# Kernel tuning notes

Measured on AMD Instinct MI355X. Metric: run time of the kernel, lower is better.

The kernel has to match this reference:

```python
import jax, jax.numpy as jnp
import numpy as np

B, S, D, H = 4, 2048, 1024, 16
DH = D // H  # attention head size = 64


def setup_inputs() -> dict:
    key = jax.random.key(0)
    ks = jax.random.split(key, 5)
    scale = 1.0 / np.sqrt(D)
    return {
        "hidden_states": jax.random.normal(ks[0], (B, S, D), dtype=jnp.float32),
        "attention_mask": jnp.zeros((B, 1, 1, S), dtype=jnp.float32),
        "Wq": jax.random.normal(ks[1], (D, D), dtype=jnp.float32) * scale,
        "bq": jnp.zeros((D,), dtype=jnp.float32),
        "Wk": jax.random.normal(ks[2], (D, D), dtype=jnp.float32) * scale,
        "bk": jnp.zeros((D,), dtype=jnp.float32),
        "Wv": jax.random.normal(ks[3], (D, D), dtype=jnp.float32) * scale,
        "bv": jnp.zeros((D,), dtype=jnp.float32),
    }


def _heads(x):
    # [B,S,D] -> [B,H,S,DH]
    return x.reshape(B, S, H, DH).transpose(0, 2, 1, 3)


def reference(hidden_states, attention_mask, Wq, bq, Wk, bk, Wv, bv):
    # QKV projections (nn.Linear: x @ W.T + b)
    q = _heads(hidden_states @ Wq.T + bq)
    k = _heads(hidden_states @ Wk.T + bk)
    v = _heads(hidden_states @ Wv.T + bv)
    # scaled dot-product attention, eval mode (no dropout, no head_mask)
    scores = jnp.einsum("bhqd,bhkd->bhqk", q, k) / np.sqrt(DH).astype(np.float32)
    scores = scores + attention_mask  # additive mask broadcast to [B,H,S,S]
    probs = jax.nn.softmax(scores, axis=-1)
    ctx = jnp.einsum("bhqk,bhkd->bhqd", probs, v)
    # [B,H,S,DH] -> [B,S,D]
    return ctx.transpose(0, 2, 1, 3).reshape(B, S, D)
```

## Files before the change

### kernel.cpp

```cpp
#include <hip/hip_runtime.h>

typedef float f32x4 __attribute__((ext_vector_type(4)));
typedef __bf16 bf16x8 __attribute__((ext_vector_type(8)));
typedef __bf16 bf16x4 __attribute__((ext_vector_type(4)));
typedef unsigned short u16;
typedef unsigned int u32;

#define SEQ 2048
#define DMODEL 1024
#define MTOT 8192
#define LOG2E 1.4426950408889634f
#define C1 0.18033688011112042f

__device__ __forceinline__ void gl_lds16(const void* g, void* l) {
  __builtin_amdgcn_global_load_lds(
      (const __attribute__((address_space(1))) u32*)g,
      (__attribute__((address_space(3))) u32*)l, 16, 0, 0);
}

__global__ __launch_bounds__(256) void cvt_kernel(
    const float* __restrict__ X, const float* __restrict__ Wq,
    const float* __restrict__ Wk, const float* __restrict__ Wv,
    const float* __restrict__ mask,
    u16* __restrict__ Xb, u16* __restrict__ Wall, float* __restrict__ mskL) {
  const long NX = (long)MTOT * DMODEL;
  const long NW = (long)DMODEL * DMODEL;
  long i = ((long)blockIdx.x * 256 + threadIdx.x) * 4;
  if (i < NX) {
    float4 v = *reinterpret_cast<const float4*>(X + i);
    bf16x4 o = {(__bf16)v.x, (__bf16)v.y, (__bf16)v.z, (__bf16)v.w};
    *reinterpret_cast<bf16x4*>(Xb + i) = o;
  } else {
    long j = i - NX;
    if (j < 3 * NW) {
      long wsel = j >> 20;
      long k = j & (NW - 1);
      const float* src = wsel == 0 ? Wq : (wsel == 1 ? Wk : Wv);
      float4 v = *reinterpret_cast<const float4*>(src + k);
      bf16x4 o = {(__bf16)v.x, (__bf16)v.y, (__bf16)v.z, (__bf16)v.w};
      *reinterpret_cast<bf16x4*>(Wall + j) = o;
    } else {
      long jm = j - 3 * NW;
      if (jm < (long)4 * SEQ) {
        float4 v = *reinterpret_cast<const float4*>(mask + jm);
        float4 o = {v.x * LOG2E, v.y * LOG2E, v.z * LOG2E, v.w * LOG2E};
        *reinterpret_cast<float4*>(mskL + jm) = o;
      }
    }
  }
}

__global__ __launch_bounds__(256) void gemm_qk(
    const u16* __restrict__ A, const u16* __restrict__ Bw,
    const float* __restrict__ bq, const float* __restrict__ bk,
    u16* __restrict__ Qb, u16* __restrict__ Kb) {
  __shared__ __align__(16) u16 As[128 * 32];
  __shared__ __align__(16) u16 Bs[128 * 32];
  const int t = threadIdx.x;
  const int l = t & 63, w = t >> 6;
  const int wr = w >> 1, wc = w & 1;
  const int g16 = l >> 4, l15 = l & 15;
  const long m0 = (long)blockIdx.x * 128;
  const long n0 = (long)blockIdx.y * 128;
  f32x4 acc[4][4] = {};

  const int rA = w * 16 + (l >> 2);
  const int cA = (l & 3) * 8;

  for (int k0 = 0; k0 < DMODEL; k0 += 32) {
#pragma unroll
    for (int is = 0; is < 2; ++is) {
      gl_lds16(A + (m0 + is * 64 + rA) * DMODEL + k0 + cA,
               (char*)As + is * 4096 + w * 1024);
      gl_lds16(Bw + (n0 + is * 64 + rA) * DMODEL + k0 + cA,
               (char*)Bs + is * 4096 + w * 1024);
    }
    __syncthreads();
    bf16x8 af[4], bf[4];
#pragma unroll
    for (int i = 0; i < 4; ++i)
      af[i] = *reinterpret_cast<const bf16x8*>(
          (const char*)As + (wr * 64 + i * 16 + l15) * 64 + g16 * 16);
#pragma unroll
    for (int j = 0; j < 4; ++j)
      bf[j] = *reinterpret_cast<const bf16x8*>(
          (const char*)Bs + (wc * 64 + j * 16 + l15) * 64 + g16 * 16);
#pragma unroll
    for (int i = 0; i < 4; ++i)
#pragma unroll
      for (int j = 0; j < 4; ++j)
        acc[i][j] = __builtin_amdgcn_mfma_f32_16x16x32_bf16(bf[j], af[i], acc[i][j], 0, 0, 0);
    __syncthreads();
  }

  const bool isQ = n0 < 1024;
  const float* bias = isQ ? bq : bk;
  u16* Cb = isQ ? Qb : Kb;
  const long nb = isQ ? n0 : n0 - 1024;
#pragma unroll
  for (int j = 0; j < 4; ++j) {
    const int nq = wc * 64 + j * 16 + g16 * 4;
    f32x4 bv4 = *reinterpret_cast<const f32x4*>(bias + nb + nq);
#pragma unroll
    for (int i = 0; i < 4; ++i) {
      const long m = m0 + wr * 64 + i * 16 + l15;
      bf16x4 pk = {(__bf16)(acc[i][j][0] + bv4[0]), (__bf16)(acc[i][j][1] + bv4[1]),
                   (__bf16)(acc[i][j][2] + bv4[2]), (__bf16)(acc[i][j][3] + bv4[3])};
      *reinterpret_cast<bf16x4*>(Cb + m * 1024 + nb + nq) = pk;
    }
  }
}

__global__ __launch_bounds__(256) void gemm_v(
    const u16* __restrict__ A, const u16* __restrict__ Bw,
    const float* __restrict__ bv, u16* __restrict__ Vt) {
  __shared__ __align__(16) u16 As[128 * 32];
  __shared__ __align__(16) u16 Bs[128 * 32];
  const int t = threadIdx.x;
  const int l = t & 63, w = t >> 6;
  const int wr = w >> 1, wc = w & 1;
  const int g16 = l >> 4, l15 = l & 15;
  const long m0 = (long)blockIdx.x * 128;
  const long n0 = (long)blockIdx.y * 128;
  f32x4 acc[4][4] = {};

  const int rA = w * 16 + (l >> 2);
  const int cA = (l & 3) * 8;

  for (int k0 = 0; k0 < DMODEL; k0 += 32) {
#pragma unroll
    for (int is = 0; is < 2; ++is) {
      gl_lds16(A + (m0 + is * 64 + rA) * DMODEL + k0 + cA,
               (char*)As + is * 4096 + w * 1024);
      gl_lds16(Bw + (n0 + is * 64 + rA) * DMODEL + k0 + cA,
               (char*)Bs + is * 4096 + w * 1024);
    }
    __syncthreads();
    bf16x8 af[4], bf[4];
#pragma unroll
    for (int i = 0; i < 4; ++i)
      af[i] = *reinterpret_cast<const bf16x8*>(
          (const char*)As + (wr * 64 + i * 16 + l15) * 64 + g16 * 16);
#pragma unroll
    for (int j = 0; j < 4; ++j)
      bf[j] = *reinterpret_cast<const bf16x8*>(
          (const char*)Bs + (wc * 64 + j * 16 + l15) * 64 + g16 * 16);
#pragma unroll
    for (int i = 0; i < 4; ++i)
#pragma unroll
      for (int j = 0; j < 4; ++j)
        acc[i][j] = __builtin_amdgcn_mfma_f32_16x16x32_bf16(af[i], bf[j], acc[i][j], 0, 0, 0);
    __syncthreads();
  }

#pragma unroll
  for (int j = 0; j < 4; ++j) {
    const int dg = (int)n0 + wc * 64 + j * 16 + l15;
    const float bias = bv[dg];
    const int h = dg >> 6, dd = dg & 63;
#pragma unroll
    for (int i = 0; i < 4; ++i) {
      const long m = m0 + wr * 64 + i * 16 + g16 * 4;
      const long b = m >> 11, s = m & 2047;
      bf16x4 pk = {(__bf16)(acc[i][j][0] + bias), (__bf16)(acc[i][j][1] + bias),
                   (__bf16)(acc[i][j][2] + bias), (__bf16)(acc[i][j][3] + bias)};
      *reinterpret_cast<bf16x4*>(Vt + ((b * 16 + h) * 64 + dd) * 2048 + s) = pk;
    }
  }
}

__global__ __launch_bounds__(256) void attn_kernel(
    const u16* __restrict__ Qb, const u16* __restrict__ Kb,
    const u16* __restrict__ Vt, const float* __restrict__ mskL,
    float* __restrict__ out) {
  __shared__ __align__(16) u16 Ks[2][64 * 64];
  __shared__ __align__(16) u16 Vs[2][64 * 64];
  __shared__ __align__(16) float Mv[2][64];
  __shared__ __align__(16) u16 Pt[4][16 * 72];

  const int qt = blockIdx.x, bh = blockIdx.y;
  const int b = bh >> 4, h = bh & 15;
  const int t = threadIdx.x, l = t & 63, w = t >> 6;
  const int l15 = l & 15, g16 = l >> 4;

  bf16x8 qf0, qf1;
  {
    const u16* Qg = Qb + ((long)b * SEQ + qt * 64 + w * 16 + l15) * 1024 + h * 64 + g16 * 8;
    qf0 = *reinterpret_cast<const bf16x8*>(Qg);
    qf1 = *reinterpret_cast<const bf16x8*>(Qg + 32);
  }

  const int swz = ((l & 7) ^ (l >> 3)) * 8;
  const u16* kp0 = Kb + ((long)b * SEQ + w * 8 + (l >> 3)) * 1024 + h * 64 + swz;
  const u16* kp1 = kp0 + (long)32 * 1024;
  const u16* vp0 = Vt + ((long)bh * 64 + w * 16 + (l >> 3)) * 2048 + swz;
  const u16* vp1 = vp0 + (long)8 * 2048;
  const float* Mg = mskL + (long)b * SEQ;

  float m_ = -INFINITY, l_ = 0.f;
  f32x4 c_[4] = {};

#define STAGE(buf, kt)                                              \
  {                                                                 \
    const long ka = (long)(kt) * 64 * 1024;                         \
    const long va = (long)(kt) * 64;                                \
    gl_lds16(kp0 + ka, Ks[buf] + w * 512);                          \
    gl_lds16(kp1 + ka, Ks[buf] + w * 512 + 2048);                   \
    gl_lds16(vp0 + va, Vs[buf] + w * 1024);                         \
    gl_lds16(vp1 + va, Vs[buf] + w * 1024 + 512);                   \
    if (t < 16) gl_lds16(Mg + (kt) * 64 + t * 4, Mv[buf]);          \
  }

  STAGE(0, 0);
  __syncthreads();

  int cb = 0;
  for (int kt = 0; kt < 32; ++kt) {
    if (kt < 31) STAGE(cb ^ 1, kt + 1);

    const char* KsB = (const char*)Ks[cb];
    const int kx0 = ((g16 ^ (l15 & 7)) & 7) << 4;
    const int kx1 = (((4 + g16) ^ (l15 & 7)) & 7) << 4;
    f32x4 s4[4] = {};
    __builtin_amdgcn_s_setprio(1);
#pragma unroll
    for (int kt16 = 0; kt16 < 4; ++kt16) {
      const char* rowp = KsB + (kt16 * 16 + l15) * 128;
      bf16x8 k0 = *reinterpret_cast<const bf16x8*>(rowp + kx0);
      bf16x8 k1 = *reinterpret_cast<const bf16x8*>(rowp + kx1);
      s4[kt16] = __builtin_amdgcn_mfma_f32_16x16x32_bf16(k0, qf0, s4[kt16], 0, 0, 0);
      s4[kt16] = __builtin_amdgcn_mfma_f32_16x16x32_bf16(k1, qf1, s4[kt16], 0, 0, 0);
    }
    __builtin_amdgcn_s_setprio(0);

    float z[16];
    float mx = -INFINITY;
#pragma unroll
    for (int kt16 = 0; kt16 < 4; ++kt16) {
      f32x4 mv4 = *reinterpret_cast<const f32x4*>(&Mv[cb][kt16 * 16 + g16 * 4]);
#pragma unroll
      for (int r = 0; r < 4; ++r) {
        const float zz = s4[kt16][r] * C1 + mv4[r];
        z[kt16 * 4 + r] = zz;
        mx = fmaxf(mx, zz);
      }
    }
    mx = fmaxf(mx, __shfl_xor(mx, 16, 64));
    mx = fmaxf(mx, __shfl_xor(mx, 32, 64));
    if (!__all(mx <= m_ + 8.0f)) {
      const float mn = fmaxf(m_, mx);
      const float sc = __builtin_amdgcn_exp2f(m_ - mn);
      m_ = mn;
      l_ *= sc;
#pragma unroll
      for (int dt = 0; dt < 4; ++dt) {
        c_[dt][0] *= sc; c_[dt][1] *= sc; c_[dt][2] *= sc; c_[dt][3] *= sc;
      }
    }
    float rs = 0.f;
#pragma unroll
    for (int i = 0; i < 16; ++i) {
      const float p = __builtin_amdgcn_exp2f(z[i] - m_);
      z[i] = p;
      rs += p;
    }
    rs += __shfl_xor(rs, 16, 64);
    rs += __shfl_xor(rs, 32, 64);
    l_ += rs;

    u16* Pw = Pt[w];
#pragma unroll
    for (int kt16 = 0; kt16 < 4; ++kt16) {
      bf16x4 pv = {(__bf16)z[kt16 * 4 + 0], (__bf16)z[kt16 * 4 + 1],
                   (__bf16)z[kt16 * 4 + 2], (__bf16)z[kt16 * 4 + 3]};
      *reinterpret_cast<bf16x4*>(Pw + l15 * 72 + kt16 * 16 + g16 * 4) = pv;
    }
    asm volatile("s_waitcnt lgkmcnt(0)" ::: "memory");
    __builtin_amdgcn_sched_barrier(0);

    const char* VsB = (const char*)Vs[cb];
    __builtin_amdgcn_s_setprio(1);
#pragma unroll
    for (int kh = 0; kh < 2; ++kh) {
      bf16x8 pb = *reinterpret_cast<const bf16x8*>(Pw + l15 * 72 + kh * 32 + g16 * 8);
#pragma unroll
      for (int dt = 0; dt < 4; ++dt) {
        const int d = dt * 16 + l15;
        bf16x8 va = *reinterpret_cast<const bf16x8*>(
            VsB + d * 128 + ((((kh * 4 + g16) ^ (d & 7)) & 7) << 4));
        c_[dt] = __builtin_amdgcn_mfma_f32_16x16x32_bf16(va, pb, c_[dt], 0, 0, 0);
      }
    }
    __builtin_amdgcn_s_setprio(0);
    __syncthreads();
    cb ^= 1;
  }

  const float inv = 1.0f / l_;
  const long orow = ((long)b * SEQ + qt * 64 + w * 16 + l15) * DMODEL + h * 64;
#pragma unroll
  for (int dt = 0; dt < 4; ++dt) {
    f32x4 o = {c_[dt][0] * inv, c_[dt][1] * inv, c_[dt][2] * inv, c_[dt][3] * inv};
    *reinterpret_cast<f32x4*>(out + orow + dt * 16 + g16 * 4) = o;
  }
}

extern "C" void kernel_launch(void* const* d_in, const int* in_sizes, int n_in,
                              void* d_out, int out_size, void* d_ws, size_t ws_size,
                              hipStream_t stream) {
  const float* X    = (const float*)d_in[0];
  const float* mask = (const float*)d_in[1];
  const float* Wq   = (const float*)d_in[2];
  const float* bq   = (const float*)d_in[3];
  const float* Wk   = (const float*)d_in[4];
  const float* bk   = (const float*)d_in[5];
  const float* Wv   = (const float*)d_in[6];
  const float* bv   = (const float*)d_in[7];
  float* out = (float*)d_out;

  char* ws = (char*)d_ws;
  u16* Xb    = (u16*)ws;
  u16* Wall  = (u16*)(ws + (16ull << 20));
  u16* Qb    = (u16*)(ws + (22ull << 20));
  u16* Kb    = (u16*)(ws + (38ull << 20));
  u16* Vt    = (u16*)(ws + (54ull << 20));
  float* mskL = (float*)(ws + (70ull << 20));

  cvt_kernel<<<11272, 256, 0, stream>>>(X, Wq, Wk, Wv, mask, Xb, Wall, mskL);
  gemm_qk<<<dim3(64, 16), 256, 0, stream>>>(Xb, Wall, bq, bk, Qb, Kb);
  gemm_v<<<dim3(64, 8), 256, 0, stream>>>(Xb, Wall + (long)2048 * 1024, bv, Vt);
  attn_kernel<<<dim3(32, 64), 256, 0, stream>>>(Qb, Kb, Vt, mskL, out);
}
```

Measured before the change: 322.7 us.

## Fuse QKV GEMMs, remap grids for XCD locality, streamline attention softmax

Merges the Q/K and V projection GEMMs into a single launch and remaps block ids so blocks on the same XCD share weight/activation tiles. The attention kernel uses a 1D grid remapped so heads cluster per XCD for L2 reuse of K/V. Mask values are prefetched into registers instead of staged through LDS, the row-max cross-lane reduction runs only when a rescale is needed, and the row-sum reduction is deferred to the end. The P tile uses an XOR swizzle instead of padding to avoid LDS bank conflicts. Adds register pressure and branch divergence in the fused GEMM.

```diff
diff --git a/kernel.cpp b/kernel.cpp
--- a/kernel.cpp
+++ b/kernel.cpp
@@ -50,29 +50,35 @@
   }
 }
 
-__global__ __launch_bounds__(256) void gemm_qk(
-    const u16* __restrict__ A, const u16* __restrict__ Bw,
+__global__ __launch_bounds__(256) void gemm_qkv(
+    const u16* __restrict__ A, const u16* __restrict__ Wall,
     const float* __restrict__ bq, const float* __restrict__ bk,
-    u16* __restrict__ Qb, u16* __restrict__ Kb) {
+    const float* __restrict__ bv,
+    u16* __restrict__ Qb, u16* __restrict__ Kb, u16* __restrict__ Vt) {
   __shared__ __align__(16) u16 As[128 * 32];
   __shared__ __align__(16) u16 Bs[128 * 32];
+  const int id = blockIdx.x;
+  const int vid = (id & 7) * 192 + (id >> 3);
+  const int bx = vid & 63, by = vid >> 6;
   const int t = threadIdx.x;
   const int l = t & 63, w = t >> 6;
   const int wr = w >> 1, wc = w & 1;
   const int g16 = l >> 4, l15 = l & 15;
-  const long m0 = (long)blockIdx.x * 128;
-  const long n0 = (long)blockIdx.y * 128;
+  const long m0 = (long)bx * 128;
+  const long n0 = (long)by * 128;
+  const bool isV = by >= 16;
   f32x4 acc[4][4] = {};
 
   const int rA = w * 16 + (l >> 2);
   const int cA = (l & 3) * 8;
+  const u16* Bw = Wall + n0 * 1024;
 
   for (int k0 = 0; k0 < DMODEL; k0 += 32) {
 #pragma unroll
     for (int is = 0; is < 2; ++is) {
       gl_lds16(A + (m0 + is * 64 + rA) * DMODEL + k0 + cA,
                (char*)As + is * 4096 + w * 1024);
-      gl_lds16(Bw + (n0 + is * 64 + rA) * DMODEL + k0 + cA,
+      gl_lds16(Bw + ((long)is * 64 + rA) * DMODEL + k0 + cA,
                (char*)Bs + is * 4096 + w * 1024);
     }
     __syncthreads();
@@ -85,86 +91,53 @@
     for (int j = 0; j < 4; ++j)
       bf[j] = *reinterpret_cast<const bf16x8*>(
           (const char*)Bs + (wc * 64 + j * 16 + l15) * 64 + g16 * 16);
-#pragma unroll
-    for (int i = 0; i < 4; ++i)
-#pragma unroll
-      for (int j = 0; j < 4; ++j)
-        acc[i][j] = __builtin_amdgcn_mfma_f32_16x16x32_bf16(bf[j], af[i], acc[i][j], 0, 0, 0);
+    if (isV) {
+#pragma unroll
+      for (int i = 0; i < 4; ++i)
+#pragma unroll
+        for (int j = 0; j < 4; ++j)
+          acc[i][j] = __builtin_amdgcn_mfma_f32_16x16x32_bf16(af[i], bf[j], acc[i][j], 0, 0, 0);
+    } else {
+#pragma unroll
+      for (int i = 0; i < 4; ++i)
+#pragma unroll
+        for (int j = 0; j < 4; ++j)
+          acc[i][j] = __builtin_amdgcn_mfma_f32_16x16x32_bf16(bf[j], af[i], acc[i][j], 0, 0, 0);
+    }
     __syncthreads();
   }
 
-  const bool isQ = n0 < 1024;
-  const float* bias = isQ ? bq : bk;
-  u16* Cb = isQ ? Qb : Kb;
-  const long nb = isQ ? n0 : n0 - 1024;
-#pragma unroll
-  for (int j = 0; j < 4; ++j) {
-    const int nq = wc * 64 + j * 16 + g16 * 4;
-    f32x4 bv4 = *reinterpret_cast<const f32x4*>(bias + nb + nq);
-#pragma unroll
-    for (int i = 0; i < 4; ++i) {
-      const long m = m0 + wr * 64 + i * 16 + l15;
-      bf16x4 pk = {(__bf16)(acc[i][j][0] + bv4[0]), (__bf16)(acc[i][j][1] + bv4[1]),
-                   (__bf16)(acc[i][j][2] + bv4[2]), (__bf16)(acc[i][j][3] + bv4[3])};
-      *reinterpret_cast<bf16x4*>(Cb + m * 1024 + nb + nq) = pk;
-    }
-  }
-}
-
-__global__ __launch_bounds__(256) void gemm_v(
-    const u16* __restrict__ A, const u16* __restrict__ Bw,
-    const float* __restrict__ bv, u16* __restrict__ Vt) {
-  __shared__ __align__(16) u16 As[128 * 32];
-  __shared__ __align__(16) u16 Bs[128 * 32];
-  const int t = threadIdx.x;
-  const int l = t & 63, w = t >> 6;
-  const int wr = w >> 1, wc = w & 1;
-  const int g16 = l >> 4, l15 = l & 15;
-  const long m0 = (long)blockIdx.x * 128;
-  const long n0 = (long)blockIdx.y * 128;
-  f32x4 acc[4][4] = {};
-
-  const int rA = w * 16 + (l >> 2);
-  const int cA = (l & 3) * 8;
-
-  for (int k0 = 0; k0 < DMODEL; k0 += 32) {
-#pragma unroll
-    for (int is = 0; is < 2; ++is) {
-      gl_lds16(A + (m0 + is * 64 + rA) * DMODEL + k0 + cA,
-               (char*)As + is * 4096 + w * 1024);
-      gl_lds16(Bw + (n0 + is * 64 + rA) * DMODEL + k0 + cA,
-               (char*)Bs + is * 4096 + w * 1024);
-    }
-    __syncthreads();
-    bf16x8 af[4], bf[4];
-#pragma unroll
-    for (int i = 0; i < 4; ++i)
-      af[i] = *reinterpret_cast<const bf16x8*>(
-          (const char*)As + (wr * 64 + i * 16 + l15) * 64 + g16 * 16);
-#pragma unroll
-    for (int j = 0; j < 4; ++j)
-      bf[j] = *reinterpret_cast<const bf16x8*>(
-          (const char*)Bs + (wc * 64 + j * 16 + l15) * 64 + g16 * 16);
-#pragma unroll
-    for (int i = 0; i < 4; ++i)
-#pragma unroll
-      for (int j = 0; j < 4; ++j)
-        acc[i][j] = __builtin_amdgcn_mfma_f32_16x16x32_bf16(af[i], bf[j], acc[i][j], 0, 0, 0);
-    __syncthreads();
-  }
-
-#pragma unroll
-  for (int j = 0; j < 4; ++j) {
-    const int dg = (int)n0 + wc * 64 + j * 16 + l15;
-    const float bias = bv[dg];
-    const int h = dg >> 6, dd = dg & 63;
-#pragma unroll
-    for (int i = 0; i < 4; ++i) {
-      const long m = m0 + wr * 64 + i * 16 + g16 * 4;
-      const long b = m >> 11, s = m & 2047;
-      bf16x4 pk = {(__bf16)(acc[i][j][0] + bias), (__bf16)(acc[i][j][1] + bias),
-                   (__bf16)(acc[i][j][2] + bias), (__bf16)(acc[i][j][3] + bias)};
-      *reinterpret_cast<bf16x4*>(Vt + ((b * 16 + h) * 64 + dd) * 2048 + s) = pk;
+  if (!isV) {
+    const bool isQ = n0 < 1024;
+    const float* bias = isQ ? bq : bk;
+    u16* Cb = isQ ? Qb : Kb;
+    const long nb = isQ ? n0 : n0 - 1024;
+#pragma unroll
+    for (int j = 0; j < 4; ++j) {
+      const int nq = wc * 64 + j * 16 + g16 * 4;
+      f32x4 bv4 = *reinterpret_cast<const f32x4*>(bias + nb + nq);
+#pragma unroll
+      for (int i = 0; i < 4; ++i) {
+        const long m = m0 + wr * 64 + i * 16 + l15;
+        bf16x4 pk = {(__bf16)(acc[i][j][0] + bv4[0]), (__bf16)(acc[i][j][1] + bv4[1]),
+                     (__bf16)(acc[i][j][2] + bv4[2]), (__bf16)(acc[i][j][3] + bv4[3])};
+        *reinterpret_cast<bf16x4*>(Cb + m * 1024 + nb + nq) = pk;
+      }
+    }
+  } else {
+#pragma unroll
+    for (int j = 0; j < 4; ++j) {
+      const int dg = (int)(n0 - 2048) + wc * 64 + j * 16 + l15;
+      const float bias = bv[dg];
+      const int h = dg >> 6, dd = dg & 63;
+#pragma unroll
+      for (int i = 0; i < 4; ++i) {
+        const long m = m0 + wr * 64 + i * 16 + g16 * 4;
+        const long b = m >> 11, s = m & 2047;
+        bf16x4 pk = {(__bf16)(acc[i][j][0] + bias), (__bf16)(acc[i][j][1] + bias),
+                     (__bf16)(acc[i][j][2] + bias), (__bf16)(acc[i][j][3] + bias)};
+        *reinterpret_cast<bf16x4*>(Vt + ((b * 16 + h) * 64 + dd) * 2048 + s) = pk;
+      }
     }
   }
 }
@@ -175,10 +148,11 @@
     float* __restrict__ out) {
   __shared__ __align__(16) u16 Ks[2][64 * 64];
   __shared__ __align__(16) u16 Vs[2][64 * 64];
-  __shared__ __align__(16) float Mv[2][64];
-  __shared__ __align__(16) u16 Pt[4][16 * 72];
-
-  const int qt = blockIdx.x, bh = blockIdx.y;
+  __shared__ __align__(16) u16 Pt[4][16 * 64];
+
+  const int id = blockIdx.x;
+  const int bh = (id & 7) * 8 + (id >> 8);
+  const int qt = (id >> 3) & 31;
   const int b = bh >> 4, h = bh & 15;
   const int t = threadIdx.x, l = t & 63, w = t >> 6;
   const int l15 = l & 15, g16 = l >> 4;
@@ -199,6 +173,7 @@
 
   float m_ = -INFINITY, l_ = 0.f;
   f32x4 c_[4] = {};
+  f32x4 mreg[4], mnext[4];
 
 #define STAGE(buf, kt)                                              \
   {                                                                 \
@@ -208,15 +183,22 @@
     gl_lds16(kp1 + ka, Ks[buf] + w * 512 + 2048);                   \
     gl_lds16(vp0 + va, Vs[buf] + w * 1024);                         \
     gl_lds16(vp1 + va, Vs[buf] + w * 1024 + 512);                   \
-    if (t < 16) gl_lds16(Mg + (kt) * 64 + t * 4, Mv[buf]);          \
   }
 
   STAGE(0, 0);
+#pragma unroll
+  for (int kt16 = 0; kt16 < 4; ++kt16)
+    mreg[kt16] = *reinterpret_cast<const f32x4*>(Mg + kt16 * 16 + g16 * 4);
   __syncthreads();
 
   int cb = 0;
   for (int kt = 0; kt < 32; ++kt) {
-    if (kt < 31) STAGE(cb ^ 1, kt + 1);
+    if (kt < 31) {
+      STAGE(cb ^ 1, kt + 1);
+#pragma unroll
+      for (int kt16 = 0; kt16 < 4; ++kt16)
+        mnext[kt16] = *reinterpret_cast<const f32x4*>(Mg + (kt + 1) * 64 + kt16 * 16 + g16 * 4);
+    }
 
     const char* KsB = (const char*)Ks[cb];
     const int kx0 = ((g16 ^ (l15 & 7)) & 7) << 4;
@@ -236,18 +218,16 @@
     float z[16];
     float mx = -INFINITY;
 #pragma unroll
-    for (int kt16 = 0; kt16 < 4; ++kt16) {
-      f32x4 mv4 = *reinterpret_cast<const f32x4*>(&Mv[cb][kt16 * 16 + g16 * 4]);
+    for (int kt16 = 0; kt16 < 4; ++kt16)
 #pragma unroll
       for (int r = 0; r < 4; ++r) {
-        const float zz = s4[kt16][r] * C1 + mv4[r];
+        const float zz = s4[kt16][r] * C1 + mreg[kt16][r];
         z[kt16 * 4 + r] = zz;
         mx = fmaxf(mx, zz);
       }
-    }
-    mx = fmaxf(mx, __shfl_xor(mx, 16, 64));
-    mx = fmaxf(mx, __shfl_xor(mx, 32, 64));
     if (!__all(mx <= m_ + 8.0f)) {
+      mx = fmaxf(mx, __shfl_xor(mx, 16, 64));
+      mx = fmaxf(mx, __shfl_xor(mx, 32, 64));
       const float mn = fmaxf(m_, mx);
       const float sc = __builtin_amdgcn_exp2f(m_ - mn);
       m_ = mn;
@@ -264,16 +244,15 @@
       z[i] = p;
       rs += p;
     }
-    rs += __shfl_xor(rs, 16, 64);
-    rs += __shfl_xor(rs, 32, 64);
     l_ += rs;
 
-    u16* Pw = Pt[w];
+    char* Pw = (char*)Pt[w];
 #pragma unroll
     for (int kt16 = 0; kt16 < 4; ++kt16) {
       bf16x4 pv = {(__bf16)z[kt16 * 4 + 0], (__bf16)z[kt16 * 4 + 1],
                    (__bf16)z[kt16 * 4 + 2], (__bf16)z[kt16 * 4 + 3]};
-      *reinterpret_cast<bf16x4*>(Pw + l15 * 72 + kt16 * 16 + g16 * 4) = pv;
+      *reinterpret_cast<bf16x4*>(
+          Pw + l15 * 128 + ((((kt16 * 2 + (g16 >> 1)) ^ (l15 & 7)) & 7) << 4) + (g16 & 1) * 8) = pv;
     }
     asm volatile("s_waitcnt lgkmcnt(0)" ::: "memory");
     __builtin_amdgcn_sched_barrier(0);
@@ -282,7 +261,8 @@
     __builtin_amdgcn_s_setprio(1);
 #pragma unroll
     for (int kh = 0; kh < 2; ++kh) {
-      bf16x8 pb = *reinterpret_cast<const bf16x8*>(Pw + l15 * 72 + kh * 32 + g16 * 8);
+      bf16x8 pb = *reinterpret_cast<const bf16x8*>(
+          Pw + l15 * 128 + ((((kh * 4 + g16) ^ (l15 & 7)) & 7) << 4));
 #pragma unroll
       for (int dt = 0; dt < 4; ++dt) {
         const int d = dt * 16 + l15;
@@ -292,10 +272,15 @@
       }
     }
     __builtin_amdgcn_s_setprio(0);
+
+#pragma unroll
+    for (int kt16 = 0; kt16 < 4; ++kt16) mreg[kt16] = mnext[kt16];
     __syncthreads();
     cb ^= 1;
   }
 
+  l_ += __shfl_xor(l_, 16, 64);
+  l_ += __shfl_xor(l_, 32, 64);
   const float inv = 1.0f / l_;
   const long orow = ((long)b * SEQ + qt * 64 + w * 16 + l15) * DMODEL + h * 64;
 #pragma unroll
@@ -327,7 +312,6 @@
   float* mskL = (float*)(ws + (70ull << 20));
 
   cvt_kernel<<<11272, 256, 0, stream>>>(X, Wq, Wk, Wv, mask, Xb, Wall, mskL);
-  gemm_qk<<<dim3(64, 16), 256, 0, stream>>>(Xb, Wall, bq, bk, Qb, Kb);
-  gemm_v<<<dim3(64, 8), 256, 0, stream>>>(Xb, Wall + (long)2048 * 1024, bv, Vt);
-  attn_kernel<<<dim3(32, 64), 256, 0, stream>>>(Qb, Kb, Vt, mskL, out);
-}
+  gemm_qkv<<<1536, 256, 0, stream>>>(Xb, Wall, bq, bk, bv, Qb, Kb, Vt);
+  attn_kernel<<<2048, 256, 0, stream>>>(Qb, Kb, Vt, mskL, out);
+}
```

Result: faster. 302.9 us (-6.1%).
